# Performance work log

Measured on AMD Instinct MI355X. Metric: run time of the kernel, lower is better.

## Reference

```python
import jax, jax.numpy as jnp
import numpy as np

N, DIM = 8192, 128

def setup_inputs() -> dict:
    key = jax.random.key(0)
    k1, k2, k3 = jax.random.split(key, 3)
    latent = jax.random.normal(k1, (N, DIM), dtype=jnp.float32)
    coords = jax.random.normal(k2, (N, 3), dtype=jnp.float32) * 5.0  # protein-scale spread
    alpha = jax.random.uniform(k3, (N,), dtype=jnp.float32)  # valid exponent range
    return {"latent": latent, "coords": coords, "alpha": alpha}

def _pairwise_dist(coords):
    # Euclidean cdist without materializing [N,N,3]
    sq = jnp.sum(coords * coords, axis=-1)  # [N]
    d2 = sq[:, None] + sq[None, :] - 2.0 * (coords @ coords.T)  # [N,N]
    return jnp.sqrt(jnp.maximum(d2, 1e-12))

def reference(latent, coords, alpha):
    D = _pairwise_dist(coords) + 1e-6  # [N,N]
    a = 0.5 * (alpha[:, None] + alpha[None, :])  # [N,N]
    # torch.no_grad() block -> stop_gradient on the clamped distance base
    D_safe = jax.lax.stop_gradient(jnp.clip(D, 1e-6, None))
    K = jnp.clip(D_safe ** (-a), 1e-8, 1000.0) * jnp.exp(-D / 12.0)
    K = jnp.clip(K, 0.0, 1000.0)
    n = K.shape[0]
    K = K * (1.0 - jnp.eye(n, dtype=K.dtype))  # fill_diagonal_(0)
    K = K / (jnp.sum(K, axis=-1, keepdims=True) + 1e-8)  # row-normalize
    out = K @ latent  # [N,DIM] aggregation
    return out, K
```

## Files before the change

### kernel.cpp

```cpp
#include <hip/hip_runtime.h>
#include <hip/hip_bf16.h>

constexpr int kN = 8192;
constexpr int kD = 128;
constexpr int BM = 32;
constexpr int BK = 64;
constexpr int JSPLIT = 8;
constexpr int LDB = 66;
constexpr int TB = 64;
constexpr int NB = kN / TB;

typedef __bf16 v8bf __attribute__((ext_vector_type(8)));
typedef float  v4f  __attribute__((ext_vector_type(4)));

__device__ __forceinline__ void gload16(const void* g, void* l) {
    __builtin_amdgcn_global_load_lds(
        (const __attribute__((address_space(1))) void*)g,
        (__attribute__((address_space(3))) void*)l, 16, 0, 0);
}

__device__ __forceinline__ float kraw_f(float4 ci, float sqi, float4 cj, float sqj) {
    float d2 = sqi + sqj - 2.0f * (ci.x * cj.x + ci.y * cj.y + ci.z * cj.z);
    d2 = fmaxf(d2, 1e-12f);
    float Dd = __builtin_amdgcn_sqrtf(d2);
    float a = 0.5f * (ci.w + cj.w);
    float t = a * (-0.5f * __builtin_amdgcn_logf(d2));
    t = fminf(fmaxf(t, -26.575424759098897f), 9.965784284662087f);
    float K = __builtin_amdgcn_exp2f(fmaf(Dd, -0.12022458674074695f, t));
    return fminf(K, 1000.0f);
}

__global__ void pack_k(const float* __restrict__ coords, const float* __restrict__ alpha,
                       float4* __restrict__ c4) {
    int j = blockIdx.x * 256 + threadIdx.x;
    if (j < kN) {
        c4[j] = make_float4(coords[3 * j], coords[3 * j + 1], coords[3 * j + 2], alpha[j]);
    }
}

__global__ void transpose_k(const float* __restrict__ latent, __bf16* __restrict__ latT) {
    __shared__ float tile[32][33];
    int t = threadIdx.x;
    int tx = t & 31, ty = t >> 5;
    int j0 = blockIdx.x * 32, d0 = blockIdx.y * 32;
    #pragma unroll
    for (int i = 0; i < 32; i += 8)
        tile[ty + i][tx] = latent[(size_t)(j0 + ty + i) * kD + d0 + tx];
    __syncthreads();
    #pragma unroll
    for (int i = 0; i < 32; i += 8)
        latT[(size_t)(d0 + ty + i) * kN + j0 + tx] = (__bf16)tile[tx][ty + i];
}

__global__ __launch_bounds__(256) void rowsum_sym_k(const float4* __restrict__ c4,
                                                    float* __restrict__ rsum) {
    __shared__ float4 rc4[TB];
    __shared__ float  rsq[TB];
    __shared__ float  rowbuf[TB][TB + 1];

    int L = blockIdx.x;
    int bi = (int)((2 * NB + 1 - sqrtf((float)((2 * NB + 1) * (2 * NB + 1) - 8 * L))) * 0.5f);
    #pragma unroll
    for (int f = 0; f < 2; ++f) {
        int s0 = bi * NB - bi * (bi - 1) / 2;
        int s1 = (bi + 1) * NB - (bi + 1) * bi / 2;
        if (L >= s1) ++bi;
        else if (L < s0) --bi;
    }
    int sbi = bi * NB - bi * (bi - 1) / 2;
    int bj = bi + (L - sbi);
    bool diag = (bi == bj);

    const int t = threadIdx.x;
    const int l = t & 63;
    const int w = t >> 6;

    if (t < TB) {
        float4 ci = c4[bi * TB + t];
        rc4[t] = ci;
        rsq[t] = ci.x * ci.x + ci.y * ci.y + ci.z * ci.z;
    }
    __syncthreads();

    float4 cj = c4[bj * TB + l];
    float sqj = cj.x * cj.x + cj.y * cj.y + cj.z * cj.z;

    float colacc = 0.f;
    #pragma unroll
    for (int rr = 0; rr < 16; ++rr) {
        int r = w * 16 + rr;
        float k = kraw_f(rc4[r], rsq[r], cj, sqj);
        if (diag && r == l) k = 0.f;
        colacc += k;
        rowbuf[r][l] = k;
    }
    __syncthreads();

    {
        int r = t >> 2, q = t & 3;
        float p = 0.f;
        #pragma unroll
        for (int m = 0; m < 16; ++m) p += rowbuf[r][q * 16 + m];
        p += __shfl_xor(p, 1, 64);
        p += __shfl_xor(p, 2, 64);
        if (q == 0) atomicAdd(&rsum[bi * TB + r], p);
    }
    if (!diag) atomicAdd(&rsum[bj * TB + l], colacc);
}

__global__ __launch_bounds__(256, 2) void main_k(
    const float4* __restrict__ c4, const float* __restrict__ rsum,
    const __bf16* __restrict__ latT, float* __restrict__ outp, float* __restrict__ Kout) {

    __shared__ __bf16 Alds[BM][LDB];
    __shared__ __bf16 Blin[kD * BK];
    __shared__ float4 c4row[BM];
    __shared__ float  sqrow[BM];
    __shared__ float  invrow[BM];

    const int t = threadIdx.x;
    const int i0 = blockIdx.x * BM;
    const int jstrip = blockIdx.y * (kN / JSPLIT);

    if (t < BM) {
        float4 ci = c4[i0 + t];
        c4row[t] = ci;
        sqrow[t] = ci.x * ci.x + ci.y * ci.y + ci.z * ci.z;
        invrow[t] = 1.0f / (rsum[i0 + t] + 1e-8f);
    }
    __syncthreads();

    const int lane = t & 63;
    const int wave = t >> 6;

    const int c2 = t & 31;
    const int rb = (t >> 5) * 4;

    float4 rc[4]; float rs[4], rv[4];
    #pragma unroll
    for (int rr = 0; rr < 4; ++rr) {
        rc[rr] = c4row[rb + rr];
        rs[rr] = sqrow[rb + rr];
        rv[rr] = invrow[rb + rr];
    }

    const int arow = lane & 15;
    const int koff = (lane >> 4) * 8;
    const int dbase = wave * 32;
    const int bswz = ((dbase + arow) & 7) << 4;

    const int srow = t >> 3;
    const int scolb = ((t & 7) ^ (srow & 7)) << 4;

    v4f acc[2][2];
    #pragma unroll
    for (int rt = 0; rt < 2; ++rt)
        #pragma unroll
        for (int dt = 0; dt < 2; ++dt) acc[rt][dt] = (v4f){0.f, 0.f, 0.f, 0.f};

    for (int cb = 0; cb < kN / JSPLIT / BK; ++cb) {
        const int j0 = jstrip + cb * BK;

        #pragma unroll
        for (int it = 0; it < 4; ++it) {
            int row = it * 32 + srow;
            const char* src = (const char*)latT + ((size_t)row * kN + j0) * 2 + scolb;
            char* dst = (char*)Blin + it * 4096 + t * 16;
            gload16(src, dst);
        }

        const int gjA = j0 + 2 * c2, gjB = gjA + 1;
        const float4 cjA = c4[gjA];
        const float4 cjB = c4[gjB];
        const float sqA = cjA.x * cjA.x + cjA.y * cjA.y + cjA.z * cjA.z;
        const float sqB = cjB.x * cjB.x + cjB.y * cjB.y + cjB.z * cjB.z;
        #pragma unroll
        for (int rr = 0; rr < 4; ++rr) {
            int r = rb + rr, gi = i0 + r;
            float kA = (gi == gjA) ? 0.0f : kraw_f(rc[rr], rs[rr], cjA, sqA);
            float kB = (gi == gjB) ? 0.0f : kraw_f(rc[rr], rs[rr], cjB, sqB);
            float knA = kA * rv[rr];
            float knB = kB * rv[rr];
            float2 st = {knA, knB};
            *reinterpret_cast<float2*>(Kout + (size_t)gi * kN + gjA) = st;
            __bf16 hA = (__bf16)knA, hB = (__bf16)knB;
            unsigned pk = ((unsigned)*(unsigned short*)&hB << 16) | *(unsigned short*)&hA;
            *reinterpret_cast<unsigned*>(&Alds[r][2 * c2]) = pk;
        }
        __syncthreads();

        #pragma unroll
        for (int kk = 0; kk < 2; ++kk) {
            v8bf a0 = *reinterpret_cast<const v8bf*>(&Alds[arow][kk * 32 + koff]);
            v8bf a1 = *reinterpret_cast<const v8bf*>(&Alds[16 + arow][kk * 32 + koff]);
            const int bc = kk * 64 + koff * 2;
            const char* bp0 = (const char*)Blin + (dbase + arow) * 128 + (bc ^ bswz);
            const char* bp1 = (const char*)Blin + (dbase + 16 + arow) * 128 + (bc ^ bswz);
            v8bf b0 = *reinterpret_cast<const v8bf*>(bp0);
            v8bf b1 = *reinterpret_cast<const v8bf*>(bp1);
            acc[0][0] = __builtin_amdgcn_mfma_f32_16x16x32_bf16(a0, b0, acc[0][0], 0, 0, 0);
            acc[0][1] = __builtin_amdgcn_mfma_f32_16x16x32_bf16(a0, b1, acc[0][1], 0, 0, 0);
            acc[1][0] = __builtin_amdgcn_mfma_f32_16x16x32_bf16(a1, b0, acc[1][0], 0, 0, 0);
            acc[1][1] = __builtin_amdgcn_mfma_f32_16x16x32_bf16(a1, b1, acc[1][1], 0, 0, 0);
        }
        __syncthreads();
    }

    const int row = (lane >> 4) * 4;
    const int col0 = wave * 32 + (lane & 15);
    #pragma unroll
    for (int rt = 0; rt < 2; ++rt)
        #pragma unroll
        for (int dt = 0; dt < 2; ++dt)
            #pragma unroll
            for (int q = 0; q < 4; ++q)
                atomicAdd(&outp[(size_t)(i0 + rt * 16 + row + q) * kD + col0 + dt * 16],
                          acc[rt][dt][q]);
}

extern "C" void kernel_launch(void* const* d_in, const int* in_sizes, int n_in,
                              void* d_out, int out_size, void* d_ws, size_t ws_size,
                              hipStream_t stream) {
    const float* latent = (const float*)d_in[0];
    const float* coords = (const float*)d_in[1];
    const float* alpha  = (const float*)d_in[2];

    float* outp = (float*)d_out;
    float* Kout = (float*)d_out + (size_t)kN * kD;

    char* ws = (char*)d_ws;
    __bf16* latT = (__bf16*)ws;
    float4* c4   = (float4*)(ws + 2u * 1024 * 1024);
    float*  rsum = (float*)(ws + 2u * 1024 * 1024 + 128 * 1024);

    hipMemsetAsync(outp, 0, (size_t)kN * kD * sizeof(float), stream);
    hipMemsetAsync(rsum, 0, kN * sizeof(float), stream);

    pack_k<<<dim3(kN / 256), dim3(256), 0, stream>>>(coords, alpha, c4);
    transpose_k<<<dim3(kN / 32, kD / 32), dim3(256), 0, stream>>>(latent, latT);
    rowsum_sym_k<<<dim3(NB * (NB + 1) / 2), dim3(256), 0, stream>>>(c4, rsum);
    main_k<<<dim3(kN / BM, JSPLIT), dim3(256), 0, stream>>>(c4, rsum, latT, outp, Kout);
}
```

Baseline: 123.8 us.

## Double-buffer A/B tiles in main kernel with smaller column step

The main kernel now keeps two LDS buffers for the K tile and the latent tile and halves the column step to 32. The next step's K values and async latent load are issued before the MFMAs on the current buffer, which leaves one barrier per iteration instead of two. The aim is to overlap kernel-value computation and global loads with matrix work and cut synchronisation stalls. In exchange the loop runs twice as many iterations with fewer MFMAs each, and the XOR swizzle on the B tile is dropped, which can cause LDS bank conflicts.

Measured after the change: 128.1 us. 3.5% more time.

```diff
diff --git a/kernel.cpp b/kernel.cpp
--- a/kernel.cpp
+++ b/kernel.cpp
@@ -4,9 +4,9 @@
 constexpr int kN = 8192;
 constexpr int kD = 128;
 constexpr int BM = 32;
-constexpr int BK = 64;
+constexpr int BW = 32;
 constexpr int JSPLIT = 8;
-constexpr int LDB = 66;
+constexpr int LDA = 40;
 constexpr int TB = 64;
 constexpr int NB = kN / TB;
 
@@ -112,15 +112,18 @@
     const float4* __restrict__ c4, const float* __restrict__ rsum,
     const __bf16* __restrict__ latT, float* __restrict__ outp, float* __restrict__ Kout) {
 
-    __shared__ __bf16 Alds[BM][LDB];
-    __shared__ __bf16 Blin[kD * BK];
+    __shared__ __bf16 Blin[2][kD][BW];
+    __shared__ __bf16 Alds[2][BM][LDA];
     __shared__ float4 c4row[BM];
     __shared__ float  sqrow[BM];
     __shared__ float  invrow[BM];
 
     const int t = threadIdx.x;
+    const int lane = t & 63;
+    const int wave = t >> 6;
     const int i0 = blockIdx.x * BM;
     const int jstrip = blockIdx.y * (kN / JSPLIT);
+    constexpr int NIT = (kN / JSPLIT) / BW;
 
     if (t < BM) {
         float4 ci = c4[i0 + t];
@@ -130,27 +133,22 @@
     }
     __syncthreads();
 
-    const int lane = t & 63;
-    const int wave = t >> 6;
-
-    const int c2 = t & 31;
-    const int rb = (t >> 5) * 4;
-
-    float4 rc[4]; float rs[4], rv[4];
-    #pragma unroll
-    for (int rr = 0; rr < 4; ++rr) {
+    const int c2 = t & 15;
+    const int rb = (t >> 4) * 2;
+    float4 rc[2]; float rs[2], rv[2];
+    #pragma unroll
+    for (int rr = 0; rr < 2; ++rr) {
         rc[rr] = c4row[rb + rr];
         rs[rr] = sqrow[rb + rr];
         rv[rr] = invrow[rb + rr];
     }
 
     const int arow = lane & 15;
-    const int koff = (lane >> 4) * 8;
+    const int slot = lane >> 4;
     const int dbase = wave * 32;
-    const int bswz = ((dbase + arow) & 7) << 4;
-
-    const int srow = t >> 3;
-    const int scolb = ((t & 7) ^ (srow & 7)) << 4;
+
+    const int srow = t >> 2;
+    const int scol = (t & 3) * 16;
 
     v4f acc[2][2];
     #pragma unroll
@@ -158,25 +156,23 @@
         #pragma unroll
         for (int dt = 0; dt < 2; ++dt) acc[rt][dt] = (v4f){0.f, 0.f, 0.f, 0.f};
 
-    for (int cb = 0; cb < kN / JSPLIT / BK; ++cb) {
-        const int j0 = jstrip + cb * BK;
-
-        #pragma unroll
-        for (int it = 0; it < 4; ++it) {
-            int row = it * 32 + srow;
-            const char* src = (const char*)latT + ((size_t)row * kN + j0) * 2 + scolb;
-            char* dst = (char*)Blin + it * 4096 + t * 16;
+    auto prepare = [&](int W, int pb) {
+        const int j0 = jstrip + W * BW;
+        #pragma unroll
+        for (int it = 0; it < 2; ++it) {
+            int row = it * 64 + srow;
+            const char* src = (const char*)latT + ((size_t)row * kN + j0) * 2 + scol;
+            char* dst = (char*)&Blin[pb][0][0] + it * 4096 + t * 16;
             gload16(src, dst);
         }
-
         const int gjA = j0 + 2 * c2, gjB = gjA + 1;
         const float4 cjA = c4[gjA];
         const float4 cjB = c4[gjB];
         const float sqA = cjA.x * cjA.x + cjA.y * cjA.y + cjA.z * cjA.z;
         const float sqB = cjB.x * cjB.x + cjB.y * cjB.y + cjB.z * cjB.z;
         #pragma unroll
-        for (int rr = 0; rr < 4; ++rr) {
-            int r = rb + rr, gi = i0 + r;
+        for (int rr = 0; rr < 2; ++rr) {
+            int gi = i0 + rb + rr;
             float kA = (gi == gjA) ? 0.0f : kraw_f(rc[rr], rs[rr], cjA, sqA);
             float kB = (gi == gjB) ? 0.0f : kraw_f(rc[rr], rs[rr], cjB, sqB);
             float knA = kA * rv[rr];
@@ -185,24 +181,26 @@
             *reinterpret_cast<float2*>(Kout + (size_t)gi * kN + gjA) = st;
             __bf16 hA = (__bf16)knA, hB = (__bf16)knB;
             unsigned pk = ((unsigned)*(unsigned short*)&hB << 16) | *(unsigned short*)&hA;
-            *reinterpret_cast<unsigned*>(&Alds[r][2 * c2]) = pk;
+            *reinterpret_cast<unsigned*>(&Alds[pb][rb + rr][2 * c2]) = pk;
         }
-        __syncthreads();
-
-        #pragma unroll
-        for (int kk = 0; kk < 2; ++kk) {
-            v8bf a0 = *reinterpret_cast<const v8bf*>(&Alds[arow][kk * 32 + koff]);
-            v8bf a1 = *reinterpret_cast<const v8bf*>(&Alds[16 + arow][kk * 32 + koff]);
-            const int bc = kk * 64 + koff * 2;
-            const char* bp0 = (const char*)Blin + (dbase + arow) * 128 + (bc ^ bswz);
-            const char* bp1 = (const char*)Blin + (dbase + 16 + arow) * 128 + (bc ^ bswz);
-            v8bf b0 = *reinterpret_cast<const v8bf*>(bp0);
-            v8bf b1 = *reinterpret_cast<const v8bf*>(bp1);
-            acc[0][0] = __builtin_amdgcn_mfma_f32_16x16x32_bf16(a0, b0, acc[0][0], 0, 0, 0);
-            acc[0][1] = __builtin_amdgcn_mfma_f32_16x16x32_bf16(a0, b1, acc[0][1], 0, 0, 0);
-            acc[1][0] = __builtin_amdgcn_mfma_f32_16x16x32_bf16(a1, b0, acc[1][0], 0, 0, 0);
-            acc[1][1] = __builtin_amdgcn_mfma_f32_16x16x32_bf16(a1, b1, acc[1][1], 0, 0, 0);
-        }
+    };
+
+    prepare(0, 0);
+    __syncthreads();
+
+    for (int cb = 0; cb < NIT; ++cb) {
+        const int p = cb & 1;
+        if (cb + 1 < NIT) prepare(cb + 1, p ^ 1);
+
+        v8bf a0 = *reinterpret_cast<const v8bf*>(&Alds[p][arow][slot * 8]);
+        v8bf a1 = *reinterpret_cast<const v8bf*>(&Alds[p][16 + arow][slot * 8]);
+        v8bf b0 = *reinterpret_cast<const v8bf*>(&Blin[p][dbase + arow][slot * 8]);
+        v8bf b1 = *reinterpret_cast<const v8bf*>(&Blin[p][dbase + 16 + arow][slot * 8]);
+        acc[0][0] = __builtin_amdgcn_mfma_f32_16x16x32_bf16(a0, b0, acc[0][0], 0, 0, 0);
+        acc[0][1] = __builtin_amdgcn_mfma_f32_16x16x32_bf16(a0, b1, acc[0][1], 0, 0, 0);
+        acc[1][0] = __builtin_amdgcn_mfma_f32_16x16x32_bf16(a1, b0, acc[1][0], 0, 0, 0);
+        acc[1][1] = __builtin_amdgcn_mfma_f32_16x16x32_bf16(a1, b1, acc[1][1], 0, 0, 0);
+
         __syncthreads();
     }
 
```
